# Kernel optimization log

Measured on AMD Instinct MI355X. Metric: run time of the kernel, lower is better.

Reference implementation:

```python
import jax, jax.numpy as jnp
import numpy as np

HEADS = 8  # head_count from init_kwargs

def _conv1x1(x, W, b):
    # x: [B,C,H,W], W: [Cout,Cin], b: [Cout] -> [B,Cout,H,W]
    return jnp.einsum('bchw,kc->bkhw', x, W) + b[None, :, None, None]

def setup_inputs() -> dict:
    key = jax.random.key(0)
    ks = jax.random.split(key, 9)
    B, C, H, W = 16, 128, 128, 128
    KC, VC = 128, 128
    s = 0.05
    return {
        'x':  jax.random.normal(ks[0], (B, C, H, W), dtype=jnp.float32),
        'Wk': jax.random.normal(ks[1], (KC, C), dtype=jnp.float32) * s,
        'bk': jnp.zeros((KC,), dtype=jnp.float32),
        'Wq': jax.random.normal(ks[2], (KC, C), dtype=jnp.float32) * s,
        'bq': jnp.zeros((KC,), dtype=jnp.float32),
        'Wv': jax.random.normal(ks[3], (VC, C), dtype=jnp.float32) * s,
        'bv': jnp.zeros((VC,), dtype=jnp.float32),
        'Wr': jax.random.normal(ks[4], (C, VC), dtype=jnp.float32) * s,
        'br': jnp.zeros((C,), dtype=jnp.float32),
    }

def reference(x, Wk, bk, Wq, bq, Wv, bv, Wr, br):
    B, C, H, W = x.shape
    N = H * W
    KC, VC = Wk.shape[0], Wv.shape[0]
    dk, dv = KC // HEADS, VC // HEADS

    keys = _conv1x1(x, Wk, bk).reshape(B, HEADS, dk, N)
    queries = _conv1x1(x, Wq, bq).reshape(B, HEADS, dk, N)
    values = _conv1x1(x, Wv, bv).reshape(B, HEADS, dv, N)

    k = jax.nn.softmax(keys, axis=-1)      # softmax over spatial positions
    q = jax.nn.softmax(queries, axis=2)    # softmax over per-head key channels

    # context: [B,h,dk,dv] = sum_n k[b,h,k,n] * v[b,h,v,n]
    context = jnp.einsum('bhkn,bhvn->bhkv', k, values)
    # attended: [B,h,dv,N] = context^T @ q
    attended = jnp.einsum('bhkv,bhkn->bhvn', context, q)
    aggregated = attended.reshape(B, VC, H, W)

    reprojected = _conv1x1(aggregated, Wr, br)
    return reprojected + x
```

## Files before the change

kernel.cpp:

```cpp
#include <hip/hip_runtime.h>
#include <hip/hip_bf16.h>

#define BATCH 16
#define CH    128
#define NPIX  16384
#define NHEAD 8

typedef __attribute__((ext_vector_type(8))) short bf16x8;
typedef __attribute__((ext_vector_type(4))) float f32x4;

__device__ __forceinline__ short f2b(float f) {
    union { float f; unsigned u; } v; v.f = f;
    unsigned r = v.u + 0x7fffu + ((v.u >> 16) & 1u);
    return (short)(r >> 16);
}

__device__ __forceinline__ int xswz(int p, int c) {
    const int v = ((p >> 2) & 15) ^ ((p & 3) << 2);
    return (p * CH + c) ^ (v << 3);
}

__device__ __forceinline__ void stage_x(const float* __restrict__ xb, int p0,
                                        ushort* lds, int tid) {
    #pragma unroll
    for (int i = 0; i < 8; ++i) {
        const int idx = tid + i * 256;
        const int c   = idx >> 4;
        const int L   = idx & 15;
        const float4 v4 = *(const float4*)(xb + (size_t)c * NPIX + p0 + L * 4);
        #pragma unroll
        for (int kk = 0; kk < 4; ++kk) {
            const int p = L * 4 + kk;
            lds[xswz(p, c)] = (ushort)f2b(((const float*)&v4)[kk]);
        }
    }
}

__global__ __launch_bounds__(256)
void k1_context(const float* __restrict__ x,
                const float* __restrict__ Wk, const float* __restrict__ bk,
                const float* __restrict__ Wv, const float* __restrict__ bv,
                float* __restrict__ Sg, float* __restrict__ Zg)
{
    __shared__ __align__(16) ushort xlds[64 * CH];

    const int tid  = threadIdx.x;
    const int w    = tid >> 6;
    const int lane = tid & 63;
    const int lo   = lane & 15;
    const int hi   = lane >> 4;

    const int b     = blockIdx.x >> 6;
    const int chunk = blockIdx.x & 63;
    const float* xb = x + (size_t)b * CH * NPIX;

    bf16x8 wkf[2][4], wvf[2][4];
    #pragma unroll
    for (int ct = 0; ct < 2; ++ct) {
        const int row = 32*w + ct*16 + lo;
        #pragma unroll
        for (int ks = 0; ks < 4; ++ks) {
            const int c0 = ks*32 + hi*8;
            const float* pk = Wk + row*CH + c0;
            const float* pv = Wv + row*CH + c0;
            bf16x8 fk, fv;
            #pragma unroll
            for (int j = 0; j < 8; ++j) { fk[j] = f2b(pk[j]); fv[j] = f2b(pv[j]); }
            wkf[ct][ks] = fk; wvf[ct][ks] = fv;
        }
    }
    float bkv[2], bvv[2];
    #pragma unroll
    for (int ct = 0; ct < 2; ++ct) {
        bkv[ct] = bk[32*w + ct*16 + lo];
        bvv[ct] = bv[32*w + ct*16 + lo];
    }

    const f32x4 zero4 = {0.f, 0.f, 0.f, 0.f};
    f32x4 sacc[2] = {zero4, zero4};
    float zacc[2] = {0.f, 0.f};

    for (int sub = 0; sub < 4; ++sub) {
        const int p0 = chunk*256 + sub*64;
        __syncthreads();
        stage_x(xb, p0, xlds, tid);
        __syncthreads();

        f32x4 dk_[2][4], dv_[2][4];
        #pragma unroll
        for (int ct = 0; ct < 2; ++ct)
            #pragma unroll
            for (int pt = 0; pt < 4; ++pt) { dk_[ct][pt] = zero4; dv_[ct][pt] = zero4; }

        #pragma unroll
        for (int ks = 0; ks < 4; ++ks) {
            #pragma unroll
            for (int pt = 0; pt < 4; ++pt) {
                const bf16x8 xa = *(const bf16x8*)&xlds[xswz(pt*16 + lo, ks*32 + hi*8)];
                #pragma unroll
                for (int ct = 0; ct < 2; ++ct) {
                    dk_[ct][pt] = __builtin_amdgcn_mfma_f32_16x16x32_bf16(xa, wkf[ct][ks], dk_[ct][pt], 0, 0, 0);
                    dv_[ct][pt] = __builtin_amdgcn_mfma_f32_16x16x32_bf16(xa, wvf[ct][ks], dv_[ct][pt], 0, 0, 0);
                }
            }
        }

        #pragma unroll
        for (int ct = 0; ct < 2; ++ct) {
            bf16x8 ef[2], vf[2];
            #pragma unroll
            for (int pt = 0; pt < 4; ++pt) {
                #pragma unroll
                for (int r = 0; r < 4; ++r) {
                    float e = __expf(dk_[ct][pt][r] + bkv[ct]);
                    zacc[ct] += e;
                    ef[pt >> 1][(pt & 1)*4 + r] = f2b(e);
                    vf[pt >> 1][(pt & 1)*4 + r] = f2b(dv_[ct][pt][r] + bvv[ct]);
                }
            }
            #pragma unroll
            for (int kg = 0; kg < 2; ++kg)
                sacc[ct] = __builtin_amdgcn_mfma_f32_16x16x32_bf16(ef[kg], vf[kg], sacc[ct], 0, 0, 0);
        }
    }

    #pragma unroll
    for (int ct = 0; ct < 2; ++ct) {
        float z = zacc[ct];
        z += __shfl_xor(z, 16, 64);
        z += __shfl_xor(z, 32, 64);
        if (hi == 0)
            atomicAdd(&Zg[b*CH + 32*w + ct*16 + lo], z);
        float* sp = Sg + (size_t)(b*NHEAD + 2*w + ct) * 256;
        #pragma unroll
        for (int r = 0; r < 4; ++r)
            atomicAdd(&sp[(hi*4 + r)*16 + lo], sacc[ct][r]);
    }
}

__global__ __launch_bounds__(256)
void k15_meff(const float* __restrict__ Sg, const float* __restrict__ Zg,
              const float* __restrict__ Wr, float* __restrict__ Meff)
{
    const int b   = blockIdx.x >> 6;
    const int idx = (blockIdx.x & 63) * 256 + threadIdx.x;
    const int c   = idx >> 7;
    const int kcg = idx & 127;
    const int h   = kcg >> 4;
    const int kc  = kcg & 15;
    const float* sp = Sg + ((size_t)(b*NHEAD + h) * 16 + kc) * 16;
    const float* wr = Wr + (size_t)c * CH + h*16;
    float acc = 0.f;
    #pragma unroll
    for (int v = 0; v < 16; ++v) acc += wr[v] * sp[v];
    Meff[((size_t)b*CH + c)*CH + kcg] = acc / Zg[b*CH + kcg];
}

__global__ __launch_bounds__(256)
void k2_out(const float* __restrict__ x,
            const float* __restrict__ Wq, const float* __restrict__ bq,
            const float* __restrict__ Meff, const float* __restrict__ br,
            float* __restrict__ out)
{
    __shared__ __align__(16) ushort xlds[64 * CH];
    __shared__ __align__(16) ushort qlds[64 * CH];

    const int tid  = threadIdx.x;
    const int w    = tid >> 6;
    const int lane = tid & 63;
    const int lo   = lane & 15;
    const int hi   = lane >> 4;

    const int b     = blockIdx.x >> 6;
    const int chunk = blockIdx.x & 63;
    const size_t xbase = (size_t)b * CH * NPIX;
    const float* xb = x + xbase;

    bf16x8 wqf[2][4], mf[2][4];
    #pragma unroll
    for (int ct = 0; ct < 2; ++ct) {
        const int row = 32*w + ct*16 + lo;
        #pragma unroll
        for (int ks = 0; ks < 4; ++ks) {
            const int c0 = ks*32 + hi*8;
            const float* pq = Wq + row*CH + c0;
            const float* pm = Meff + ((size_t)b*CH + row)*CH + c0;
            bf16x8 fq, fm;
            #pragma unroll
            for (int j = 0; j < 8; ++j) { fq[j] = f2b(pq[j]); fm[j] = f2b(pm[j]); }
            wqf[ct][ks] = fq; mf[ct][ks] = fm;
        }
    }
    float bqv[2];
    #pragma unroll
    for (int ct = 0; ct < 2; ++ct) bqv[ct] = bq[32*w + ct*16 + lo];
    float brv[2][4];
    #pragma unroll
    for (int ct = 0; ct < 2; ++ct)
        #pragma unroll
        for (int r = 0; r < 4; ++r) brv[ct][r] = br[32*w + ct*16 + hi*4 + r];

    const f32x4 zero4 = {0.f, 0.f, 0.f, 0.f};

    for (int sub = 0; sub < 4; ++sub) {
        const int p0 = chunk*256 + sub*64;
        __syncthreads();
        stage_x(xb, p0, xlds, tid);
        __syncthreads();

        f32x4 dq[2][4];
        #pragma unroll
        for (int ct = 0; ct < 2; ++ct)
            #pragma unroll
            for (int pt = 0; pt < 4; ++pt) dq[ct][pt] = zero4;

        #pragma unroll
        for (int ks = 0; ks < 4; ++ks) {
            #pragma unroll
            for (int pt = 0; pt < 4; ++pt) {
                const bf16x8 xa = *(const bf16x8*)&xlds[xswz(pt*16 + lo, ks*32 + hi*8)];
                #pragma unroll
                for (int ct = 0; ct < 2; ++ct)
                    dq[ct][pt] = __builtin_amdgcn_mfma_f32_16x16x32_bf16(xa, wqf[ct][ks], dq[ct][pt], 0, 0, 0);
            }
        }

        #pragma unroll
        for (int ct = 0; ct < 2; ++ct) {
            const int qc = 32*w + ct*16 + lo;
            #pragma unroll
            for (int pt = 0; pt < 4; ++pt) {
                #pragma unroll
                for (int r = 0; r < 4; ++r) {
                    const float e = __expf(dq[ct][pt][r] + bqv[ct]);
                    float s = e;
                    s += __shfl_xor(s, 1, 64);
                    s += __shfl_xor(s, 2, 64);
                    s += __shfl_xor(s, 4, 64);
                    s += __shfl_xor(s, 8, 64);
                    const float q = e / s;
                    const int pos = pt*16 + hi*4 + r;
                    const int sidx = (pos*CH + qc) ^ ((pos & 7) << 3);
                    qlds[sidx] = (ushort)f2b(q);
                }
            }
        }
        __syncthreads();

        f32x4 d2[2][4];
        #pragma unroll
        for (int ct = 0; ct < 2; ++ct)
            #pragma unroll
            for (int pt = 0; pt < 4; ++pt) d2[ct][pt] = zero4;

        #pragma unroll
        for (int ks = 0; ks < 4; ++ks) {
            #pragma unroll
            for (int pt = 0; pt < 4; ++pt) {
                const int pos  = pt*16 + lo;
                const int sidx = (pos*CH + ks*32 + hi*8) ^ ((pos & 7) << 3);
                const bf16x8 qf = *(const bf16x8*)&qlds[sidx];
                #pragma unroll
                for (int ct = 0; ct < 2; ++ct)
                    d2[ct][pt] = __builtin_amdgcn_mfma_f32_16x16x32_bf16(mf[ct][ks], qf, d2[ct][pt], 0, 0, 0);
            }
        }

        #pragma unroll
        for (int ct = 0; ct < 2; ++ct)
            #pragma unroll
            for (int pt = 0; pt < 4; ++pt) {
                const int n   = p0 + pt*16 + lo;
                const int pos = pt*16 + lo;
                #pragma unroll
                for (int r = 0; r < 4; ++r) {
                    const int cc = 32*w + ct*16 + hi*4 + r;
                    union { unsigned u; float f; } xr;
                    xr.u = ((unsigned)xlds[xswz(pos, cc)]) << 16;
                    out[xbase + (size_t)cc * NPIX + n] = d2[ct][pt][r] + brv[ct][r] + xr.f;
                }
            }
    }
}

extern "C" void kernel_launch(void* const* d_in, const int* in_sizes, int n_in,
                              void* d_out, int out_size, void* d_ws, size_t ws_size,
                              hipStream_t stream)
{
    const float* x  = (const float*)d_in[0];
    const float* Wk = (const float*)d_in[1];
    const float* bk = (const float*)d_in[2];
    const float* Wq = (const float*)d_in[3];
    const float* bq = (const float*)d_in[4];
    const float* Wv = (const float*)d_in[5];
    const float* bv = (const float*)d_in[6];
    const float* Wr = (const float*)d_in[7];
    const float* br = (const float*)d_in[8];
    float* out = (float*)d_out;

    float* Sg   = (float*)d_ws;
    float* Zg   = Sg + 32768;
    float* Meff = Zg + 2048;

    hipMemsetAsync(d_ws, 0, (32768 + 2048) * sizeof(float), stream);

    k1_context<<<dim3(BATCH * 64), dim3(256), 0, stream>>>(x, Wk, bk, Wv, bv, Sg, Zg);
    k15_meff  <<<dim3(BATCH * 64), dim3(256), 0, stream>>>(Sg, Zg, Wr, Meff);
    k2_out    <<<dim3(BATCH * 64), dim3(256), 0, stream>>>(x, Wq, bq, Meff, br, out);
}
```

Before: 442.9 us.

## Prefetch x into registers, replace atomics with partial-sum reduction, coalesce output stores

```diff
diff --git a/kernel.cpp b/kernel.cpp
--- a/kernel.cpp
+++ b/kernel.cpp
@@ -14,33 +14,20 @@
     unsigned r = v.u + 0x7fffu + ((v.u >> 16) & 1u);
     return (short)(r >> 16);
 }
+__device__ __forceinline__ float b2f(ushort u) {
+    union { unsigned u; float f; } v; v.u = ((unsigned)u) << 16; return v.f;
+}
 
 __device__ __forceinline__ int xswz(int p, int c) {
     const int v = ((p >> 2) & 15) ^ ((p & 3) << 2);
     return (p * CH + c) ^ (v << 3);
-}
-
-__device__ __forceinline__ void stage_x(const float* __restrict__ xb, int p0,
-                                        ushort* lds, int tid) {
-    #pragma unroll
-    for (int i = 0; i < 8; ++i) {
-        const int idx = tid + i * 256;
-        const int c   = idx >> 4;
-        const int L   = idx & 15;
-        const float4 v4 = *(const float4*)(xb + (size_t)c * NPIX + p0 + L * 4);
-        #pragma unroll
-        for (int kk = 0; kk < 4; ++kk) {
-            const int p = L * 4 + kk;
-            lds[xswz(p, c)] = (ushort)f2b(((const float*)&v4)[kk]);
-        }
-    }
 }
 
 __global__ __launch_bounds__(256)
 void k1_context(const float* __restrict__ x,
                 const float* __restrict__ Wk, const float* __restrict__ bk,
                 const float* __restrict__ Wv, const float* __restrict__ bv,
-                float* __restrict__ Sg, float* __restrict__ Zg)
+                float* __restrict__ Sp, float* __restrict__ Zp)
 {
     __shared__ __align__(16) ushort xlds[64 * CH];
 
@@ -54,6 +41,17 @@
     const int chunk = blockIdx.x & 63;
     const float* xb = x + (size_t)b * CH * NPIX;
 
+    const int pc = tid >> 4;
+    const int pL = tid & 15;
+
+    float4 pf[8];
+    {
+        const int p0 = chunk * 256;
+        #pragma unroll
+        for (int i = 0; i < 8; ++i)
+            pf[i] = *(const float4*)(xb + (size_t)(pc + 16*i) * NPIX + p0 + pL * 4);
+    }
+
     bf16x8 wkf[2][4], wvf[2][4];
     #pragma unroll
     for (int ct = 0; ct < 2; ++ct) {
@@ -61,11 +59,15 @@
         #pragma unroll
         for (int ks = 0; ks < 4; ++ks) {
             const int c0 = ks*32 + hi*8;
-            const float* pk = Wk + row*CH + c0;
-            const float* pv = Wv + row*CH + c0;
+            const float4 k0 = *(const float4*)(Wk + row*CH + c0);
+            const float4 k1 = *(const float4*)(Wk + row*CH + c0 + 4);
+            const float4 v0 = *(const float4*)(Wv + row*CH + c0);
+            const float4 v1 = *(const float4*)(Wv + row*CH + c0 + 4);
             bf16x8 fk, fv;
-            #pragma unroll
-            for (int j = 0; j < 8; ++j) { fk[j] = f2b(pk[j]); fv[j] = f2b(pv[j]); }
+            fk[0]=f2b(k0.x); fk[1]=f2b(k0.y); fk[2]=f2b(k0.z); fk[3]=f2b(k0.w);
+            fk[4]=f2b(k1.x); fk[5]=f2b(k1.y); fk[6]=f2b(k1.z); fk[7]=f2b(k1.w);
+            fv[0]=f2b(v0.x); fv[1]=f2b(v0.y); fv[2]=f2b(v0.z); fv[3]=f2b(v0.w);
+            fv[4]=f2b(v1.x); fv[5]=f2b(v1.y); fv[6]=f2b(v1.z); fv[7]=f2b(v1.w);
             wkf[ct][ks] = fk; wvf[ct][ks] = fv;
         }
     }
@@ -80,49 +82,62 @@
     f32x4 sacc[2] = {zero4, zero4};
     float zacc[2] = {0.f, 0.f};
 
+    #pragma unroll
     for (int sub = 0; sub < 4; ++sub) {
-        const int p0 = chunk*256 + sub*64;
-        __syncthreads();
-        stage_x(xb, p0, xlds, tid);
-        __syncthreads();
-
-        f32x4 dk_[2][4], dv_[2][4];
-        #pragma unroll
-        for (int ct = 0; ct < 2; ++ct)
-            #pragma unroll
-            for (int pt = 0; pt < 4; ++pt) { dk_[ct][pt] = zero4; dv_[ct][pt] = zero4; }
-
-        #pragma unroll
-        for (int ks = 0; ks < 4; ++ks) {
-            #pragma unroll
-            for (int pt = 0; pt < 4; ++pt) {
-                const bf16x8 xa = *(const bf16x8*)&xlds[xswz(pt*16 + lo, ks*32 + hi*8)];
-                #pragma unroll
-                for (int ct = 0; ct < 2; ++ct) {
-                    dk_[ct][pt] = __builtin_amdgcn_mfma_f32_16x16x32_bf16(xa, wkf[ct][ks], dk_[ct][pt], 0, 0, 0);
-                    dv_[ct][pt] = __builtin_amdgcn_mfma_f32_16x16x32_bf16(xa, wvf[ct][ks], dv_[ct][pt], 0, 0, 0);
+        #pragma unroll
+        for (int i = 0; i < 8; ++i) {
+            const int c = pc + 16*i;
+            #pragma unroll
+            for (int kk = 0; kk < 4; ++kk)
+                xlds[xswz(pL*4 + kk, c)] = (ushort)f2b(((const float*)&pf[i])[kk]);
+        }
+        __syncthreads();
+
+        if (sub < 3) {
+            const int pn = chunk*256 + (sub+1)*64;
+            #pragma unroll
+            for (int i = 0; i < 8; ++i)
+                pf[i] = *(const float4*)(xb + (size_t)(pc + 16*i) * NPIX + pn + pL * 4);
+        }
+
+        #pragma unroll
+        for (int ct = 0; ct < 2; ++ct) {
+            f32x4 dk_[4], dv_[4];
+            #pragma unroll
+            for (int pt = 0; pt < 4; ++pt) { dk_[pt] = zero4; dv_[pt] = zero4; }
+            #pragma unroll
+            for (int ks = 0; ks < 4; ++ks) {
+                #pragma unroll
+                for (int pt = 0; pt < 4; ++pt) {
+                    const bf16x8 xa = *(const bf16x8*)&xlds[xswz(pt*16 + lo, ks*32 + hi*8)];
+                    dk_[pt] = __builtin_amdgcn_mfma_f32_16x16x32_bf16(xa, wkf[ct][ks], dk_[pt], 0, 0, 0);
+                    dv_[pt] = __builtin_amdgcn_mfma_f32_16x16x32_bf16(xa, wvf[ct][ks], dv_[pt], 0, 0, 0);
                 }
             }
-        }
-
-        #pragma unroll
-        for (int ct = 0; ct < 2; ++ct) {
             bf16x8 ef[2], vf[2];
             #pragma unroll
             for (int pt = 0; pt < 4; ++pt) {
                 #pragma unroll
                 for (int r = 0; r < 4; ++r) {
-                    float e = __expf(dk_[ct][pt][r] + bkv[ct]);
+                    float e = __expf(dk_[pt][r] + bkv[ct]);
                     zacc[ct] += e;
                     ef[pt >> 1][(pt & 1)*4 + r] = f2b(e);
-                    vf[pt >> 1][(pt & 1)*4 + r] = f2b(dv_[ct][pt][r] + bvv[ct]);
+                    vf[pt >> 1][(pt & 1)*4 + r] = f2b(dv_[pt][r] + bvv[ct]);
                 }
             }
             #pragma unroll
             for (int kg = 0; kg < 2; ++kg)
                 sacc[ct] = __builtin_amdgcn_mfma_f32_16x16x32_bf16(ef[kg], vf[kg], sacc[ct], 0, 0, 0);
         }
-    }
+        __syncthreads();
+    }
+
+    float* sp = Sp + (size_t)(b*64 + chunk) * 2048;
+    #pragma unroll
+    for (int ct = 0; ct < 2; ++ct)
+        #pragma unroll
+        for (int r = 0; r < 4; ++r)
+            sp[(2*w + ct)*256 + (hi*4 + r)*16 + lo] = sacc[ct][r];
 
     #pragma unroll
     for (int ct = 0; ct < 2; ++ct) {
@@ -130,17 +145,35 @@
         z += __shfl_xor(z, 16, 64);
         z += __shfl_xor(z, 32, 64);
         if (hi == 0)
-            atomicAdd(&Zg[b*CH + 32*w + ct*16 + lo], z);
-        float* sp = Sg + (size_t)(b*NHEAD + 2*w + ct) * 256;
-        #pragma unroll
-        for (int r = 0; r < 4; ++r)
-            atomicAdd(&sp[(hi*4 + r)*16 + lo], sacc[ct][r]);
+            Zp[(size_t)(b*64 + chunk) * 128 + 32*w + ct*16 + lo] = z;
+    }
+}
+
+__global__ __launch_bounds__(256)
+void k1b_reduce(const float* __restrict__ Sp, const float* __restrict__ Zp,
+                float* __restrict__ Sg, float* __restrict__ Zg)
+{
+    const int b = blockIdx.y;
+    const int j = blockIdx.x * 256 + threadIdx.x;
+    if (j < 2048) {
+        const float* p = Sp + (size_t)b * 64 * 2048 + j;
+        float a = 0.f;
+        #pragma unroll 8
+        for (int c = 0; c < 64; ++c) a += p[(size_t)c * 2048];
+        Sg[b*2048 + j] = a;
+    } else if (j < 2176) {
+        const int k = j - 2048;
+        const float* p = Zp + (size_t)b * 64 * 128 + k;
+        float a = 0.f;
+        #pragma unroll 8
+        for (int c = 0; c < 64; ++c) a += p[(size_t)c * 128];
+        Zg[b*128 + k] = a;
     }
 }
 
 __global__ __launch_bounds__(256)
 void k15_meff(const float* __restrict__ Sg, const float* __restrict__ Zg,
-              const float* __restrict__ Wr, float* __restrict__ Meff)
+              const float* __restrict__ Wr, ushort* __restrict__ Meffh)
 {
     const int b   = blockIdx.x >> 6;
     const int idx = (blockIdx.x & 63) * 256 + threadIdx.x;
@@ -148,22 +181,27 @@
     const int kcg = idx & 127;
     const int h   = kcg >> 4;
     const int kc  = kcg & 15;
-    const float* sp = Sg + ((size_t)(b*NHEAD + h) * 16 + kc) * 16;
+    const float* sp = Sg + (size_t)b*2048 + h*256 + kc*16;
     const float* wr = Wr + (size_t)c * CH + h*16;
     float acc = 0.f;
     #pragma unroll
-    for (int v = 0; v < 16; ++v) acc += wr[v] * sp[v];
-    Meff[((size_t)b*CH + c)*CH + kcg] = acc / Zg[b*CH + kcg];
+    for (int v4i = 0; v4i < 4; ++v4i) {
+        const float4 sv = *(const float4*)(sp + v4i*4);
+        const float4 wv = *(const float4*)(wr + v4i*4);
+        acc += sv.x*wv.x + sv.y*wv.y + sv.z*wv.z + sv.w*wv.w;
+    }
+    Meffh[((size_t)b*CH + c)*CH + kcg] = (ushort)f2b(acc / Zg[b*128 + kcg]);
 }
 
 __global__ __launch_bounds__(256)
 void k2_out(const float* __restrict__ x,
             const float* __restrict__ Wq, const float* __restrict__ bq,
-            const float* __restrict__ Meff, const float* __restrict__ br,
+            const ushort* __restrict__ Meffh, const float* __restrict__ br,
             float* __restrict__ out)
 {
     __shared__ __align__(16) ushort xlds[64 * CH];
     __shared__ __align__(16) ushort qlds[64 * CH];
+    __shared__ __align__(16) ushort ylds[64 * CH];
 
     const int tid  = threadIdx.x;
     const int w    = tid >> 6;
@@ -175,6 +213,18 @@
     const int chunk = blockIdx.x & 63;
     const size_t xbase = (size_t)b * CH * NPIX;
     const float* xb = x + xbase;
+    float* outb = out + xbase;
+
+    const int pc = tid >> 4;
+    const int pL = tid & 15;
+
+    float4 pf[8];
+    {
+        const int p0 = chunk * 256;
+        #pragma unroll
+        for (int i = 0; i < 8; ++i)
+            pf[i] = *(const float4*)(xb + (size_t)(pc + 16*i) * NPIX + p0 + pL * 4);
+    }
 
     bf16x8 wqf[2][4], mf[2][4];
     #pragma unroll
@@ -183,37 +233,49 @@
         #pragma unroll
         for (int ks = 0; ks < 4; ++ks) {
             const int c0 = ks*32 + hi*8;
-            const float* pq = Wq + row*CH + c0;
-            const float* pm = Meff + ((size_t)b*CH + row)*CH + c0;
-            bf16x8 fq, fm;
-            #pragma unroll
-            for (int j = 0; j < 8; ++j) { fq[j] = f2b(pq[j]); fm[j] = f2b(pm[j]); }
-            wqf[ct][ks] = fq; mf[ct][ks] = fm;
+            const float4 q0 = *(const float4*)(Wq + row*CH + c0);
+            const float4 q1 = *(const float4*)(Wq + row*CH + c0 + 4);
+            bf16x8 fq;
+            fq[0]=f2b(q0.x); fq[1]=f2b(q0.y); fq[2]=f2b(q0.z); fq[3]=f2b(q0.w);
+            fq[4]=f2b(q1.x); fq[5]=f2b(q1.y); fq[6]=f2b(q1.z); fq[7]=f2b(q1.w);
+            wqf[ct][ks] = fq;
+            mf[ct][ks] = *(const bf16x8*)(Meffh + ((size_t)b*CH + row)*CH + c0);
         }
     }
     float bqv[2];
     #pragma unroll
     for (int ct = 0; ct < 2; ++ct) bqv[ct] = bq[32*w + ct*16 + lo];
-    float brv[2][4];
-    #pragma unroll
-    for (int ct = 0; ct < 2; ++ct)
-        #pragma unroll
-        for (int r = 0; r < 4; ++r) brv[ct][r] = br[32*w + ct*16 + hi*4 + r];
+    float brv2[8];
+    #pragma unroll
+    for (int i = 0; i < 8; ++i) brv2[i] = br[pc + 16*i];
 
     const f32x4 zero4 = {0.f, 0.f, 0.f, 0.f};
 
+    #pragma unroll
     for (int sub = 0; sub < 4; ++sub) {
         const int p0 = chunk*256 + sub*64;
-        __syncthreads();
-        stage_x(xb, p0, xlds, tid);
-        __syncthreads();
+
+        #pragma unroll
+        for (int i = 0; i < 8; ++i) {
+            const int c = pc + 16*i;
+            #pragma unroll
+            for (int kk = 0; kk < 4; ++kk)
+                xlds[xswz(pL*4 + kk, c)] = (ushort)f2b(((const float*)&pf[i])[kk]);
+        }
+        __syncthreads();
+
+        if (sub < 3) {
+            const int pn = chunk*256 + (sub+1)*64;
+            #pragma unroll
+            for (int i = 0; i < 8; ++i)
+                pf[i] = *(const float4*)(xb + (size_t)(pc + 16*i) * NPIX + pn + pL * 4);
+        }
 
         f32x4 dq[2][4];
         #pragma unroll
         for (int ct = 0; ct < 2; ++ct)
             #pragma unroll
             for (int pt = 0; pt < 4; ++pt) dq[ct][pt] = zero4;
-
         #pragma unroll
         for (int ks = 0; ks < 4; ++ks) {
             #pragma unroll
@@ -252,7 +314,6 @@
         for (int ct = 0; ct < 2; ++ct)
             #pragma unroll
             for (int pt = 0; pt < 4; ++pt) d2[ct][pt] = zero4;
-
         #pragma unroll
         for (int ks = 0; ks < 4; ++ks) {
             #pragma unroll
@@ -270,16 +331,28 @@
         for (int ct = 0; ct < 2; ++ct)
             #pragma unroll
             for (int pt = 0; pt < 4; ++pt) {
-                const int n   = p0 + pt*16 + lo;
-                const int pos = pt*16 + lo;
                 #pragma unroll
                 for (int r = 0; r < 4; ++r) {
-                    const int cc = 32*w + ct*16 + hi*4 + r;
-                    union { unsigned u; float f; } xr;
-                    xr.u = ((unsigned)xlds[xswz(pos, cc)]) << 16;
-                    out[xbase + (size_t)cc * NPIX + n] = d2[ct][pt][r] + brv[ct][r] + xr.f;
+                    const int c = 32*w + ct*16 + hi*4 + r;
+                    const int e = c*64 + ((pt*16 + lo) ^ ((c & 7) << 3));
+                    ylds[e] = (ushort)f2b(d2[ct][pt][r]);
                 }
             }
+        __syncthreads();
+
+        #pragma unroll
+        for (int i = 0; i < 8; ++i) {
+            const int c = pc + 16*i;
+            const size_t g = (size_t)c * NPIX + p0 + pL * 4;
+            const float4 x4 = *(const float4*)(xb + g);
+            const ushort4 y4 = *(const ushort4*)&ylds[c*64 + 4*(pL ^ ((c & 7) << 1))];
+            float4 o;
+            o.x = b2f(y4.x) + brv2[i] + x4.x;
+            o.y = b2f(y4.y) + brv2[i] + x4.y;
+            o.z = b2f(y4.z) + brv2[i] + x4.z;
+            o.w = b2f(y4.w) + brv2[i] + x4.w;
+            *(float4*)(outb + g) = o;
+        }
     }
 }
 
@@ -298,13 +371,14 @@
     const float* br = (const float*)d_in[8];
     float* out = (float*)d_out;
 
-    float* Sg   = (float*)d_ws;
-    float* Zg   = Sg + 32768;
-    float* Meff = Zg + 2048;
-
-    hipMemsetAsync(d_ws, 0, (32768 + 2048) * sizeof(float), stream);
-
-    k1_context<<<dim3(BATCH * 64), dim3(256), 0, stream>>>(x, Wk, bk, Wv, bv, Sg, Zg);
-    k15_meff  <<<dim3(BATCH * 64), dim3(256), 0, stream>>>(Sg, Zg, Wr, Meff);
-    k2_out    <<<dim3(BATCH * 64), dim3(256), 0, stream>>>(x, Wq, bq, Meff, br, out);
-}
+    float*  Sp    = (float*)d_ws;
+    float*  Zp    = Sp + (size_t)16*64*2048;
+    float*  Sg    = Zp + (size_t)16*64*128;
+    float*  Zg    = Sg + 32768;
+    ushort* Meffh = (ushort*)(Zg + 2048);
+
+    k1_context<<<dim3(BATCH * 64), dim3(256), 0, stream>>>(x, Wk, bk, Wv, bv, Sp, Zp);
+    k1b_reduce<<<dim3(9, BATCH),   dim3(256), 0, stream>>>(Sp, Zp, Sg, Zg);
+    k15_meff  <<<dim3(BATCH * 64), dim3(256), 0, stream>>>(Sg, Zg, Wr, Meffh);
+    k2_out    <<<dim3(BATCH * 64), dim3(256), 0, stream>>>(x, Wq, bq, Meffh, br, out);
+}
```

Measured after the change: 436.1 us. About the same (-1.5%).
